# Kernel tuning notes

Hardware: AMD Instinct MI355X
Metric: run time of the kernel (lower is better)

The kernel has to match this reference:

```python
import jax, jax.numpy as jnp
import numpy as np

B, L, D, H = 4, 2048, 1024, 16
HD = D // H  # head_dim = 64


def setup_inputs() -> dict:
    key = jax.random.key(0)
    k1, k2, k3 = jax.random.split(key, 3)
    x = jax.random.normal(k1, (B, L, D), dtype=jnp.float32)
    # causal mask: True where attention is NOT allowed (masked_fill semantics)
    mask = ~jnp.tril(jnp.ones((L, L), dtype=bool))
    Wqkv = jax.random.normal(k2, (3 * D, D), dtype=jnp.float32) * (1.0 / np.sqrt(D))
    bqkv = jnp.zeros((3 * D,), dtype=jnp.float32)
    Wo = jax.random.normal(k3, (D, D), dtype=jnp.float32) * (1.0 / np.sqrt(D))
    bo = jnp.zeros((D,), dtype=jnp.float32)
    return {"x": x, "mask": mask, "Wqkv": Wqkv, "bqkv": bqkv, "Wo": Wo, "bo": bo}


def reference(x, mask, Wqkv, bqkv, Wo, bo):
    b, l, d = x.shape
    qkv = jnp.einsum('bld,ed->ble', x, Wqkv) + bqkv            # [b, l, 3d]
    q, k, v = jnp.split(qkv, 3, axis=-1)
    q = q.reshape(b, l, H, HD).transpose(0, 2, 1, 3)           # [b, h, l, hd]
    k = k.reshape(b, l, H, HD).transpose(0, 2, 1, 3)
    v = v.reshape(b, l, H, HD).transpose(0, 2, 1, 3)
    scale = 1.0 / jnp.sqrt(jnp.float32(HD))
    a = jnp.einsum('bhqd,bhkd->bhqk', q, k) * scale            # [b, h, l, l]
    a = jnp.where(mask, -jnp.inf, a)
    a = jax.nn.softmax(a, axis=-1)
    out = jnp.einsum('bhqk,bhkd->bhqd', a, v)                  # [b, h, l, hd]
    out = out.transpose(0, 2, 1, 3).reshape(b, l, d)
    return jnp.einsum('bld,ed->ble', out, Wo) + bo
```

## Files before the change

kernel.cpp:

```cpp
#include <hip/hip_runtime.h>

typedef __attribute__((ext_vector_type(8))) short short8;
typedef __attribute__((ext_vector_type(4))) float f32x4;
typedef __attribute__((ext_vector_type(16))) float f32x16;
typedef __attribute__((ext_vector_type(2))) int int2v;
typedef __attribute__((ext_vector_type(4))) int int4v;
typedef unsigned short u16;
typedef unsigned int u32;

#define B_ 4
#define L_ 2048
#define D_ 1024
#define H_ 16
#define HD_ 64

__device__ __forceinline__ void load_lds16(const void* g, void* l) {
  __builtin_amdgcn_global_load_lds(
      (__attribute__((address_space(1))) unsigned int*)(g),
      (__attribute__((address_space(3))) unsigned int*)(l),
      16, 0, 0);
}

__device__ __forceinline__ u16 f2bf(float f) {
  union { float f; unsigned u; } c; c.f = f;
  unsigned r = c.u + 0x7FFFu + ((c.u >> 16) & 1u);
  return (u16)(r >> 16);
}

__device__ __forceinline__ u32 cvtpk(float a, float b) {
  u32 r; asm("v_cvt_pk_bf16_f32 %0, %1, %2" : "=v"(r) : "v"(a), "v"(b)); return r;
}

#define TRREAD(dst, base, OFFLIT) \
  asm volatile("ds_read_b64_tr_b16 %0, %1 offset:" OFFLIT : "=v"(dst) : "v"(base))

__device__ __forceinline__ void pswap(u32& a, u32& b) {
  asm("v_permlane32_swap_b32 %0, %1" : "+v"(a), "+v"(b));
}

__global__ __launch_bounds__(256) void cvt_all(const float* __restrict__ x,
                                               const float* __restrict__ wqkv,
                                               const float* __restrict__ wo,
                                               u16* __restrict__ out) {
  const long n1 = (long)B_ * L_ * D_;
  const long n2 = (long)3 * D_ * D_;
  long i = ((long)blockIdx.x * 256 + threadIdx.x) * 4;
  const float* src;
  long off;
  if (i < n1) { src = x; off = i; }
  else if (i < n1 + n2) { src = wqkv; off = i - n1; }
  else { src = wo; off = i - n1 - n2; }
  float4 v = *(const float4*)(src + off);
  u16 o0 = f2bf(v.x), o1 = f2bf(v.y), o2 = f2bf(v.z), o3 = f2bf(v.w);
  u16* p = out + i;
  p[0] = o0; p[1] = o1; p[2] = o2; p[3] = o3;
}

template <int QCOLS, bool BF16_OUT>
__global__ __launch_bounds__(256, 3) void gemm_bt(
    const u16* __restrict__ A, const u16* __restrict__ B,
    const float* __restrict__ bias, void* __restrict__ Cout,
    int M, int N, int K) {
  __shared__ u16 Asm[128 * 64];
  __shared__ u16 Bsm[128 * 64];
  const int tid = threadIdx.x;
  const int lane = tid & 63;
  const int wid = tid >> 6;
  const int fr = lane & 15, fq = lane >> 4;
  const int wr = wid >> 1, wc = wid & 1;

  const int nwg = gridDim.x;
  const int cpx = nwg >> 3;
  const int id = (blockIdx.x & 7) * cpx + (blockIdx.x >> 3);
  const int NBX = N >> 7;
  const long n0 = (long)(id % NBX) * 128;
  const long m0 = (long)(id / NBX) * 128;

  const int srl = lane >> 3;
  const int sgc = ((lane & 7) ^ srl) * 8;

  f32x4 acc[4][4] = {};

  for (int kt = 0; kt < K; kt += 64) {
    __syncthreads();
#pragma unroll
    for (int c = 0; c < 4; ++c) {
      const int row = c * 32 + wid * 8 + srl;
      load_lds16(A + (m0 + row) * K + kt + sgc,
                 (char*)Asm + (c * 256 + wid * 64) * 16);
      load_lds16(B + (n0 + row) * K + kt + sgc,
                 (char*)Bsm + (c * 256 + wid * 64) * 16);
    }
    __syncthreads();
#pragma unroll
    for (int ks = 0; ks < 2; ++ks) {
      short8 af[4], bfr[4];
#pragma unroll
      for (int m = 0; m < 4; ++m) {
        const int row = wr * 64 + m * 16 + fr;
        af[m] = *(const short8*)((const char*)Asm + row * 128 +
                                 (((ks * 4 + fq) ^ (row & 7)) * 16));
      }
#pragma unroll
      for (int n = 0; n < 4; ++n) {
        const int row = wc * 64 + n * 16 + fr;
        bfr[n] = *(const short8*)((const char*)Bsm + row * 128 +
                                  (((ks * 4 + fq) ^ (row & 7)) * 16));
      }
#pragma unroll
      for (int m = 0; m < 4; ++m)
#pragma unroll
        for (int n = 0; n < 4; ++n)
          acc[m][n] = __builtin_amdgcn_mfma_f32_16x16x32_bf16(af[m], bfr[n], acc[m][n], 0, 0, 0);
    }
  }

  float bv[4];
#pragma unroll
  for (int n = 0; n < 4; ++n) bv[n] = bias[n0 + wc * 64 + n * 16 + fr];

#pragma unroll
  for (int m = 0; m < 4; ++m) {
#pragma unroll
    for (int n = 0; n < 4; ++n) {
      const long col = n0 + wc * 64 + n * 16 + fr;
      const float sc = (QCOLS > 0 && col < QCOLS) ? 0.18033688f : 1.0f;
#pragma unroll
      for (int r = 0; r < 4; ++r) {
        const long row = m0 + wr * 64 + m * 16 + fq * 4 + r;
        float v = (acc[m][n][r] + bv[n]) * sc;
        if (BF16_OUT)
          ((u16*)Cout)[row * N + col] = f2bf(v);
        else
          ((float*)Cout)[row * N + col] = v;
      }
    }
  }
}

__global__ __launch_bounds__(256, 4) void flash_attn11(
    const u16* __restrict__ qkv, u16* __restrict__ attn) {
  __shared__ u16 K2[2][64 * 64];
  __shared__ u16 V2[2][64 * 64];

  const int tid = threadIdx.x;
  const int lane = tid & 63;
  const int wid = tid >> 6;
  const int l31 = lane & 31;
  const int h = lane >> 5;

  const int bh = blockIdx.x;
  const int y = blockIdx.y;
  const int qt = (y < 4) ? 15 - y : (y < 8) ? y + 4 : (y < 12) ? 15 - y : y - 12;
  const long rowbase = (long)(bh >> 4) * L_;
  const int hh = bh & 15;

  const int wq0 = qt * 128 + wid * 32;
  const int qg = wq0 + l31;

  short8 qf[4];
  {
    const u16* qp = qkv + (rowbase + qg) * 3072 + hh * 64 + h * 8;
#pragma unroll
    for (int ks = 0; ks < 4; ++ks) qf[ks] = *(const short8*)(qp + ks * 16);
  }

  short8 ones;
#pragma unroll
  for (int j = 0; j < 8; ++j) ones[j] = (short)0x3F80;

  int krow[2], kvv[2], dvv[2];
#pragma unroll
  for (int c = 0; c < 2; ++c) {
    const int s = (wid * 2 + c) * 8 + (lane >> 3);
    krow[c] = s;
    kvv[c] = ((s >> 2) << 2) + ((lane >> 1) & 3);
    dvv[c] = ((s & 3) << 4) + ((lane & 1) << 3);
  }
  const int kchunk = ((lane & 7) ^ (lane >> 3)) * 8;

  const u32 Vaddr = (u32)(unsigned long long)(__attribute__((address_space(3))) char*)(void*)&V2[0][0];
  const u32 vb0 = Vaddr + ((lane >> 4) & 1) * 128 + (lane & 15) * 8 + h * 1024;

  f32x16 o[2] = {};
  float l_r = 0.f;

  auto stage = [&](int kt, int buf) {
    const long ktb = (long)kt * 64;
#pragma unroll
    for (int c = 0; c < 2; ++c) {
      load_lds16(qkv + (rowbase + ktb + krow[c]) * 3072 + 1024 + hh * 64 + kchunk,
                 (char*)&K2[buf][0] + (wid * 2 + c) * 1024);
      load_lds16(qkv + (rowbase + ktb + kvv[c]) * 3072 + 2048 + hh * 64 + dvv[c],
                 (char*)&V2[buf][0] + (wid * 2 + c) * 1024);
    }
  };

  const int ktm = 2 * qt + 1;
  stage(0, 0);
  __syncthreads();
  int cur = 0;
  for (int kt = 0; kt <= ktm; ++kt) {
    if (kt < ktm) stage(kt + 1, cur ^ 1);
    const int ktb = kt * 64;
    if (ktb <= wq0 + 31) {
      const char* Kb = (const char*)&K2[cur][0];
      const u32 vbB = vb0 + (u32)cur * 8192;

      f32x16 p[2];
      __builtin_amdgcn_s_setprio(1);
#pragma unroll
      for (int t = 0; t < 2; ++t) {
        f32x16 acc = {};
#pragma unroll
        for (int ks = 0; ks < 4; ++ks) {
          const int row = t * 32 + l31;
          short8 kf = *(const short8*)(Kb + row * 128 + (((ks * 2 + h) ^ (row & 7)) * 16));
          acc = __builtin_amdgcn_mfma_f32_32x32x16_bf16(kf, qf[ks], acc, 0, 0, 0);
        }
        p[t] = acc;
      }
      __builtin_amdgcn_s_setprio(0);

      __builtin_amdgcn_sched_barrier(0);
      int2v vf[16];
      TRREAD(vf[0], vbB, "0");     TRREAD(vf[1], vbB, "512");
      TRREAD(vf[2], vbB, "2048");  TRREAD(vf[3], vbB, "2560");
      TRREAD(vf[4], vbB, "4096");  TRREAD(vf[5], vbB, "4608");
      TRREAD(vf[6], vbB, "6144");  TRREAD(vf[7], vbB, "6656");
      TRREAD(vf[8], vbB, "256");   TRREAD(vf[9], vbB, "768");
      TRREAD(vf[10], vbB, "2304"); TRREAD(vf[11], vbB, "2816");
      TRREAD(vf[12], vbB, "4352"); TRREAD(vf[13], vbB, "4864");
      TRREAD(vf[14], vbB, "6400"); TRREAD(vf[15], vbB, "6912");

      if (ktb + 63 > wq0) {
#pragma unroll
        for (int t = 0; t < 2; ++t)
#pragma unroll
          for (int r = 0; r < 16; ++r) {
            const int kvg = ktb + t * 32 + (r & 3) + 8 * (r >> 2) + 4 * h;
            p[t][r] = (kvg > qg) ? -__builtin_inff() : p[t][r];
          }
      }

#pragma unroll
      for (int t = 0; t < 2; ++t)
#pragma unroll
        for (int r = 0; r < 16; ++r)
          p[t][r] = __builtin_exp2f(p[t][r]);

      u32 pf[4][4];
#pragma unroll
      for (int t = 0; t < 2; ++t)
#pragma unroll
        for (int ksl = 0; ksl < 2; ++ksl) {
          u32 x0 = cvtpk(p[t][8 * ksl + 0], p[t][8 * ksl + 1]);
          u32 x1 = cvtpk(p[t][8 * ksl + 2], p[t][8 * ksl + 3]);
          u32 y0 = cvtpk(p[t][8 * ksl + 4], p[t][8 * ksl + 5]);
          u32 y1 = cvtpk(p[t][8 * ksl + 6], p[t][8 * ksl + 7]);
          pswap(x0, y0);
          pswap(x1, y1);
          const int ks = t * 2 + ksl;
          pf[ks][0] = x0; pf[ks][1] = x1; pf[ks][2] = y0; pf[ks][3] = y1;
        }

      asm volatile("s_waitcnt lgkmcnt(0)" ::: "memory");
      __builtin_amdgcn_sched_barrier(0);
      __builtin_amdgcn_s_setprio(1);
      f32x16 lac = {};
#pragma unroll
      for (int ks = 0; ks < 4; ++ks) {
        int4v pv;
        pv[0] = (int)pf[ks][0]; pv[1] = (int)pf[ks][1];
        pv[2] = (int)pf[ks][2]; pv[3] = (int)pf[ks][3];
        const short8 pvf = __builtin_bit_cast(short8, pv);
        int4v a0;
        a0[0] = vf[ks * 2][0]; a0[1] = vf[ks * 2][1];
        a0[2] = vf[ks * 2 + 1][0]; a0[3] = vf[ks * 2 + 1][1];
        o[0] = __builtin_amdgcn_mfma_f32_32x32x16_bf16(
            __builtin_bit_cast(short8, a0), pvf, o[0], 0, 0, 0);
        int4v a1;
        a1[0] = vf[8 + ks * 2][0]; a1[1] = vf[8 + ks * 2][1];
        a1[2] = vf[8 + ks * 2 + 1][0]; a1[3] = vf[8 + ks * 2 + 1][1];
        o[1] = __builtin_amdgcn_mfma_f32_32x32x16_bf16(
            __builtin_bit_cast(short8, a1), pvf, o[1], 0, 0, 0);
        lac = __builtin_amdgcn_mfma_f32_32x32x16_bf16(ones, pvf, lac, 0, 0, 0);
      }
      __builtin_amdgcn_s_setprio(0);
      l_r += lac[0];
    }
    __syncthreads();
    cur ^= 1;
  }

  const float invl = 1.0f / l_r;
  u16* orow = attn + (rowbase + qg) * 1024 + hh * 64;
#pragma unroll
  for (int t = 0; t < 2; ++t)
#pragma unroll
    for (int rp = 0; rp < 8; ++rp) {
      const int r0 = rp * 2;
      const u32 w = cvtpk(o[t][r0] * invl, o[t][r0 + 1] * invl);
      const int d = t * 32 + (r0 & 3) + 8 * (r0 >> 2) + 4 * h;
      *(u32*)(orow + d) = w;
    }
}

extern "C" void kernel_launch(void* const* d_in, const int* in_sizes, int n_in,
                              void* d_out, int out_size, void* d_ws, size_t ws_size,
                              hipStream_t stream) {
  const float* x    = (const float*)d_in[0];
  const float* Wqkv = (const float*)d_in[2];
  const float* bqkv = (const float*)d_in[3];
  const float* Wo   = (const float*)d_in[4];
  const float* bo   = (const float*)d_in[5];
  float* out = (float*)d_out;

  const long ML = (long)B_ * L_;
  u16* xb    = (u16*)d_ws;
  u16* wqkvb = xb + ML * D_;
  u16* wob   = wqkvb + (long)3 * D_ * D_;
  u16* qkv   = wob + (long)D_ * D_;
  u16* attn  = qkv + ML * 3 * D_;

  const long ncvt = ML * D_ + (long)3 * D_ * D_ + (long)D_ * D_;
  cvt_all<<<dim3((int)(ncvt / 1024)), 256, 0, stream>>>(x, Wqkv, Wo, xb);

  gemm_bt<1024, true><<<dim3((3 * D_ / 128) * (int)(ML / 128)), 256, 0, stream>>>(
      xb, wqkvb, bqkv, qkv, (int)ML, 3 * D_, D_);

  flash_attn11<<<dim3(64, 16), 256, 0, stream>>>(qkv, attn);

  gemm_bt<0, false><<<dim3((D_ / 128) * (int)(ML / 128)), 256, 0, stream>>>(
      attn, wob, bo, out, (int)ML, D_, D_);
}
```

Baseline: 162.8 us.

## Software-pipeline QK^T of next tile with softmax/PV of previous tile in attention

```diff
diff --git a/kernel.cpp b/kernel.cpp
--- a/kernel.cpp
+++ b/kernel.cpp
@@ -138,10 +138,10 @@
   }
 }
 
-__global__ __launch_bounds__(256, 4) void flash_attn11(
+__global__ __launch_bounds__(256, 2) void flash_attn12(
     const u16* __restrict__ qkv, u16* __restrict__ attn) {
   __shared__ u16 K2[2][64 * 64];
-  __shared__ u16 V2[2][64 * 64];
+  __shared__ u16 V3[3][64 * 64];
 
   const int tid = threadIdx.x;
   const int lane = tid & 63;
@@ -179,121 +179,141 @@
   }
   const int kchunk = ((lane & 7) ^ (lane >> 3)) * 8;
 
-  const u32 Vaddr = (u32)(unsigned long long)(__attribute__((address_space(3))) char*)(void*)&V2[0][0];
+  const u32 Vaddr = (u32)(unsigned long long)(__attribute__((address_space(3))) char*)(void*)&V3[0][0];
   const u32 vb0 = Vaddr + ((lane >> 4) & 1) * 128 + (lane & 15) * 8 + h * 1024;
 
   f32x16 o[2] = {};
-  float l_r = 0.f;
-
-  auto stage = [&](int kt, int buf) {
+  f32x16 lacc = {};
+
+  auto stage = [&](int kt, int kbuf, int vbuf) {
     const long ktb = (long)kt * 64;
 #pragma unroll
     for (int c = 0; c < 2; ++c) {
       load_lds16(qkv + (rowbase + ktb + krow[c]) * 3072 + 1024 + hh * 64 + kchunk,
-                 (char*)&K2[buf][0] + (wid * 2 + c) * 1024);
+                 (char*)&K2[kbuf][0] + (wid * 2 + c) * 1024);
       load_lds16(qkv + (rowbase + ktb + kvv[c]) * 3072 + 2048 + hh * 64 + dvv[c],
-                 (char*)&V2[buf][0] + (wid * 2 + c) * 1024);
+                 (char*)&V3[vbuf][0] + (wid * 2 + c) * 1024);
     }
   };
 
+  auto qk_issue = [&](f32x16& W0, f32x16& W1, int kbuf) {
+    const char* Kb = (const char*)&K2[kbuf][0];
+    __builtin_amdgcn_s_setprio(1);
+#pragma unroll
+    for (int t = 0; t < 2; ++t) {
+      f32x16 acc = {};
+#pragma unroll
+      for (int ks = 0; ks < 4; ++ks) {
+        const int row = t * 32 + l31;
+        short8 kf = *(const short8*)(Kb + row * 128 + (((ks * 2 + h) ^ (row & 7)) * 16));
+        acc = __builtin_amdgcn_mfma_f32_32x32x16_bf16(kf, qf[ks], acc, 0, 0, 0);
+      }
+      if (t == 0) W0 = acc; else W1 = acc;
+    }
+    __builtin_amdgcn_s_setprio(0);
+  };
+
+  auto finish = [&](f32x16& R0, f32x16& R1, int ktbP, int vbuf) {
+    const u32 vbB = vb0 + (u32)vbuf * 8192;
+    int2v vf[16];
+    TRREAD(vf[0], vbB, "0");     TRREAD(vf[1], vbB, "512");
+    TRREAD(vf[2], vbB, "2048");  TRREAD(vf[3], vbB, "2560");
+    TRREAD(vf[4], vbB, "4096");  TRREAD(vf[5], vbB, "4608");
+    TRREAD(vf[6], vbB, "6144");  TRREAD(vf[7], vbB, "6656");
+    TRREAD(vf[8], vbB, "256");   TRREAD(vf[9], vbB, "768");
+    TRREAD(vf[10], vbB, "2304"); TRREAD(vf[11], vbB, "2816");
+    TRREAD(vf[12], vbB, "4352"); TRREAD(vf[13], vbB, "4864");
+    TRREAD(vf[14], vbB, "6400"); TRREAD(vf[15], vbB, "6912");
+
+    f32x16 p[2];
+    p[0] = R0; p[1] = R1;
+    if (ktbP + 63 > wq0) {
+#pragma unroll
+      for (int t = 0; t < 2; ++t)
+#pragma unroll
+        for (int r = 0; r < 16; ++r) {
+          const int kvg = ktbP + t * 32 + (r & 3) + 8 * (r >> 2) + 4 * h;
+          p[t][r] = (kvg > qg) ? -__builtin_inff() : p[t][r];
+        }
+    }
+#pragma unroll
+    for (int t = 0; t < 2; ++t)
+#pragma unroll
+      for (int r = 0; r < 16; ++r)
+        p[t][r] = __builtin_exp2f(p[t][r]);
+
+    u32 pf[4][4];
+#pragma unroll
+    for (int t = 0; t < 2; ++t)
+#pragma unroll
+      for (int ksl = 0; ksl < 2; ++ksl) {
+        u32 x0 = cvtpk(p[t][8 * ksl + 0], p[t][8 * ksl + 1]);
+        u32 x1 = cvtpk(p[t][8 * ksl + 2], p[t][8 * ksl + 3]);
+        u32 y0 = cvtpk(p[t][8 * ksl + 4], p[t][8 * ksl + 5]);
+        u32 y1 = cvtpk(p[t][8 * ksl + 6], p[t][8 * ksl + 7]);
+        pswap(x0, y0);
+        pswap(x1, y1);
+        const int ks = t * 2 + ksl;
+        pf[ks][0] = x0; pf[ks][1] = x1; pf[ks][2] = y0; pf[ks][3] = y1;
+      }
+
+    asm volatile("s_waitcnt lgkmcnt(0)" ::: "memory");
+    __builtin_amdgcn_sched_barrier(0);
+    __builtin_amdgcn_s_setprio(1);
+#pragma unroll
+    for (int ks = 0; ks < 4; ++ks) {
+      int4v pv;
+      pv[0] = (int)pf[ks][0]; pv[1] = (int)pf[ks][1];
+      pv[2] = (int)pf[ks][2]; pv[3] = (int)pf[ks][3];
+      const short8 pvf = __builtin_bit_cast(short8, pv);
+      int4v a0;
+      a0[0] = vf[ks * 2][0]; a0[1] = vf[ks * 2][1];
+      a0[2] = vf[ks * 2 + 1][0]; a0[3] = vf[ks * 2 + 1][1];
+      o[0] = __builtin_amdgcn_mfma_f32_32x32x16_bf16(
+          __builtin_bit_cast(short8, a0), pvf, o[0], 0, 0, 0);
+      int4v a1;
+      a1[0] = vf[8 + ks * 2][0]; a1[1] = vf[8 + ks * 2][1];
+      a1[2] = vf[8 + ks * 2 + 1][0]; a1[3] = vf[8 + ks * 2 + 1][1];
+      o[1] = __builtin_amdgcn_mfma_f32_32x32x16_bf16(
+          __builtin_bit_cast(short8, a1), pvf, o[1], 0, 0, 0);
+      lacc = __builtin_amdgcn_mfma_f32_32x32x16_bf16(ones, pvf, lacc, 0, 0, 0);
+    }
+    __builtin_amdgcn_s_setprio(0);
+  };
+
   const int ktm = 2 * qt + 1;
-  stage(0, 0);
+  stage(0, 0, 0);
   __syncthreads();
-  int cur = 0;
-  for (int kt = 0; kt <= ktm; ++kt) {
-    if (kt < ktm) stage(kt + 1, cur ^ 1);
+
+  f32x16 PA0, PA1, PB0, PB1;
+  int kt = 0, vcur = 0;
+
+  auto step = [&](f32x16& W0, f32x16& W1, f32x16& R0, f32x16& R1) {
     const int ktb = kt * 64;
-    if (ktb <= wq0 + 31) {
-      const char* Kb = (const char*)&K2[cur][0];
-      const u32 vbB = vb0 + (u32)cur * 8192;
-
-      f32x16 p[2];
-      __builtin_amdgcn_s_setprio(1);
-#pragma unroll
-      for (int t = 0; t < 2; ++t) {
-        f32x16 acc = {};
-#pragma unroll
-        for (int ks = 0; ks < 4; ++ks) {
-          const int row = t * 32 + l31;
-          short8 kf = *(const short8*)(Kb + row * 128 + (((ks * 2 + h) ^ (row & 7)) * 16));
-          acc = __builtin_amdgcn_mfma_f32_32x32x16_bf16(kf, qf[ks], acc, 0, 0, 0);
-        }
-        p[t] = acc;
-      }
-      __builtin_amdgcn_s_setprio(0);
-
-      __builtin_amdgcn_sched_barrier(0);
-      int2v vf[16];
-      TRREAD(vf[0], vbB, "0");     TRREAD(vf[1], vbB, "512");
-      TRREAD(vf[2], vbB, "2048");  TRREAD(vf[3], vbB, "2560");
-      TRREAD(vf[4], vbB, "4096");  TRREAD(vf[5], vbB, "4608");
-      TRREAD(vf[6], vbB, "6144");  TRREAD(vf[7], vbB, "6656");
-      TRREAD(vf[8], vbB, "256");   TRREAD(vf[9], vbB, "768");
-      TRREAD(vf[10], vbB, "2304"); TRREAD(vf[11], vbB, "2816");
-      TRREAD(vf[12], vbB, "4352"); TRREAD(vf[13], vbB, "4864");
-      TRREAD(vf[14], vbB, "6400"); TRREAD(vf[15], vbB, "6912");
-
-      if (ktb + 63 > wq0) {
-#pragma unroll
-        for (int t = 0; t < 2; ++t)
-#pragma unroll
-          for (int r = 0; r < 16; ++r) {
-            const int kvg = ktb + t * 32 + (r & 3) + 8 * (r >> 2) + 4 * h;
-            p[t][r] = (kvg > qg) ? -__builtin_inff() : p[t][r];
-          }
-      }
-
-#pragma unroll
-      for (int t = 0; t < 2; ++t)
-#pragma unroll
-        for (int r = 0; r < 16; ++r)
-          p[t][r] = __builtin_exp2f(p[t][r]);
-
-      u32 pf[4][4];
-#pragma unroll
-      for (int t = 0; t < 2; ++t)
-#pragma unroll
-        for (int ksl = 0; ksl < 2; ++ksl) {
-          u32 x0 = cvtpk(p[t][8 * ksl + 0], p[t][8 * ksl + 1]);
-          u32 x1 = cvtpk(p[t][8 * ksl + 2], p[t][8 * ksl + 3]);
-          u32 y0 = cvtpk(p[t][8 * ksl + 4], p[t][8 * ksl + 5]);
-          u32 y1 = cvtpk(p[t][8 * ksl + 6], p[t][8 * ksl + 7]);
-          pswap(x0, y0);
-          pswap(x1, y1);
-          const int ks = t * 2 + ksl;
-          pf[ks][0] = x0; pf[ks][1] = x1; pf[ks][2] = y0; pf[ks][3] = y1;
-        }
-
-      asm volatile("s_waitcnt lgkmcnt(0)" ::: "memory");
-      __builtin_amdgcn_sched_barrier(0);
-      __builtin_amdgcn_s_setprio(1);
-      f32x16 lac = {};
-#pragma unroll
-      for (int ks = 0; ks < 4; ++ks) {
-        int4v pv;
-        pv[0] = (int)pf[ks][0]; pv[1] = (int)pf[ks][1];
-        pv[2] = (int)pf[ks][2]; pv[3] = (int)pf[ks][3];
-        const short8 pvf = __builtin_bit_cast(short8, pv);
-        int4v a0;
-        a0[0] = vf[ks * 2][0]; a0[1] = vf[ks * 2][1];
-        a0[2] = vf[ks * 2 + 1][0]; a0[3] = vf[ks * 2 + 1][1];
-        o[0] = __builtin_amdgcn_mfma_f32_32x32x16_bf16(
-            __builtin_bit_cast(short8, a0), pvf, o[0], 0, 0, 0);
-        int4v a1;
-        a1[0] = vf[8 + ks * 2][0]; a1[1] = vf[8 + ks * 2][1];
-        a1[2] = vf[8 + ks * 2 + 1][0]; a1[3] = vf[8 + ks * 2 + 1][1];
-        o[1] = __builtin_amdgcn_mfma_f32_32x32x16_bf16(
-            __builtin_bit_cast(short8, a1), pvf, o[1], 0, 0, 0);
-        lac = __builtin_amdgcn_mfma_f32_32x32x16_bf16(ones, pvf, lac, 0, 0, 0);
-      }
-      __builtin_amdgcn_s_setprio(0);
-      l_r += lac[0];
-    }
-    __syncthreads();
-    cur ^= 1;
-  }
-
-  const float invl = 1.0f / l_r;
+    if (kt <= ktm) {
+      if (kt < ktm) {
+        const int vn = (vcur == 2) ? 0 : vcur + 1;
+        stage(kt + 1, (kt + 1) & 1, vn);
+      }
+      if (ktb <= wq0 + 31) qk_issue(W0, W1, kt & 1);
+    }
+    if (kt >= 1 && (ktb - 64) <= wq0 + 31) {
+      const int vp = (vcur == 0) ? 2 : vcur - 1;
+      finish(R0, R1, ktb - 64, vp);
+    }
+    if (kt <= ktm) __syncthreads();
+  };
+
+  while (true) {
+    step(PA0, PA1, PB0, PB1);
+    if (kt == ktm + 1) break;
+    ++kt; vcur = (vcur == 2) ? 0 : vcur + 1;
+    step(PB0, PB1, PA0, PA1);
+    if (kt == ktm + 1) break;
+    ++kt; vcur = (vcur == 2) ? 0 : vcur + 1;
+  }
+
+  const float invl = 1.0f / lacc[0];
   u16* orow = attn + (rowbase + qg) * 1024 + hh * 64;
 #pragma unroll
   for (int t = 0; t < 2; ++t)
@@ -329,7 +349,7 @@
   gemm_bt<1024, true><<<dim3((3 * D_ / 128) * (int)(ML / 128)), 256, 0, stream>>>(
       xb, wqkvb, bqkv, qkv, (int)ML, 3 * D_, D_);
 
-  flash_attn11<<<dim3(64, 16), 256, 0, stream>>>(qkv, attn);
+  flash_attn12<<<dim3(64, 16), 256, 0, stream>>>(qkv, attn);
 
   gemm_bt<0, false><<<dim3((D_ / 128) * (int)(ML / 128)), 256, 0, stream>>>(
       attn, wob, bo, out, (int)ML, D_, D_);
```

Measured after the change: 160.5 us. Within noise of the previous version (-1.4%).

## Replace direct global-to-LDS loads with register-staged prefetch in GEMM and attention

Applied to the files above, without the earlier changes.

```diff
diff --git a/kernel.cpp b/kernel.cpp
--- a/kernel.cpp
+++ b/kernel.cpp
@@ -14,12 +14,6 @@
 #define H_ 16
 #define HD_ 64
 
-__device__ __forceinline__ void load_lds16(const void* g, void* l) {
-  __builtin_amdgcn_global_load_lds(
-      (__attribute__((address_space(1))) unsigned int*)(g),
-      (__attribute__((address_space(3))) unsigned int*)(l),
-      16, 0, 0);
-}
 
 __device__ __forceinline__ u16 f2bf(float f) {
   union { float f; unsigned u; } c; c.f = f;
@@ -32,7 +26,8 @@
 }
 
 #define TRREAD(dst, base, OFFLIT) \
-  asm volatile("ds_read_b64_tr_b16 %0, %1 offset:" OFFLIT : "=v"(dst) : "v"(base))
+  asm volatile("ds_read_b64_tr_b16 %0, %1 offset:" OFFLIT \
+               : "=v"(dst) : "v"(base) : "memory")
 
 __device__ __forceinline__ void pswap(u32& a, u32& b) {
   asm("v_permlane32_swap_b32 %0, %1" : "+v"(a), "+v"(b));
@@ -79,19 +74,40 @@
   const int srl = lane >> 3;
   const int sgc = ((lane & 7) ^ srl) * 8;
 
+  const u16* gA[4];
+  const u16* gB[4];
+  u32 ldst[4];
+#pragma unroll
+  for (int c = 0; c < 4; ++c) {
+    const int row = c * 32 + wid * 8 + srl;
+    gA[c] = A + (m0 + row) * K + sgc;
+    gB[c] = B + (n0 + row) * K + sgc;
+    ldst[c] = (u32)((c * 256 + wid * 64) * 16 + lane * 16);
+  }
+
   f32x4 acc[4][4] = {};
+  short8 rA[4], rB[4];
+#pragma unroll
+  for (int c = 0; c < 4; ++c) {
+    rA[c] = *(const short8*)(gA[c]);
+    rB[c] = *(const short8*)(gB[c]);
+  }
 
   for (int kt = 0; kt < K; kt += 64) {
     __syncthreads();
 #pragma unroll
     for (int c = 0; c < 4; ++c) {
-      const int row = c * 32 + wid * 8 + srl;
-      load_lds16(A + (m0 + row) * K + kt + sgc,
-                 (char*)Asm + (c * 256 + wid * 64) * 16);
-      load_lds16(B + (n0 + row) * K + kt + sgc,
-                 (char*)Bsm + (c * 256 + wid * 64) * 16);
+      *(short8*)((char*)Asm + ldst[c]) = rA[c];
+      *(short8*)((char*)Bsm + ldst[c]) = rB[c];
     }
     __syncthreads();
+    if (kt + 64 < K) {
+#pragma unroll
+      for (int c = 0; c < 4; ++c) {
+        rA[c] = *(const short8*)(gA[c] + kt + 64);
+        rB[c] = *(const short8*)(gB[c] + kt + 64);
+      }
+    }
 #pragma unroll
     for (int ks = 0; ks < 2; ++ks) {
       short8 af[4], bfr[4];
@@ -138,10 +154,10 @@
   }
 }
 
-__global__ __launch_bounds__(256, 4) void flash_attn11(
+__global__ __launch_bounds__(256, 4) void flash_attn18(
     const u16* __restrict__ qkv, u16* __restrict__ attn) {
-  __shared__ u16 K2[2][64 * 64];
-  __shared__ u16 V2[2][64 * 64];
+  __shared__ u16 K1[64 * 64];
+  __shared__ u16 V1[64 * 64];
 
   const int tid = threadIdx.x;
   const int lane = tid & 63;
@@ -169,43 +185,53 @@
 #pragma unroll
   for (int j = 0; j < 8; ++j) ones[j] = (short)0x3F80;
 
-  int krow[2], kvv[2], dvv[2];
+  const u16* gK[2];
+  const u16* gV[2];
+  u32 dstKV[2];
 #pragma unroll
   for (int c = 0; c < 2; ++c) {
     const int s = (wid * 2 + c) * 8 + (lane >> 3);
-    krow[c] = s;
-    kvv[c] = ((s >> 2) << 2) + ((lane >> 1) & 3);
-    dvv[c] = ((s & 3) << 4) + ((lane & 1) << 3);
-  }
-  const int kchunk = ((lane & 7) ^ (lane >> 3)) * 8;
-
-  const u32 Vaddr = (u32)(unsigned long long)(__attribute__((address_space(3))) char*)(void*)&V2[0][0];
+    const int kvv = ((s >> 2) << 2) + ((lane >> 1) & 3);
+    const int dvv = ((s & 3) << 4) + ((lane & 1) << 3);
+    const int kchunk = ((lane & 7) ^ (lane >> 3)) * 8;
+    gK[c] = qkv + (rowbase + s) * 3072 + 1024 + hh * 64 + kchunk;
+    gV[c] = qkv + (rowbase + kvv) * 3072 + 2048 + hh * 64 + dvv;
+    dstKV[c] = (u32)((wid * 2 + c) * 1024 + lane * 16);
+  }
+
+  const u32 Vaddr = (u32)(unsigned long long)(__attribute__((address_space(3))) char*)(void*)&V1[0];
   const u32 vb0 = Vaddr + ((lane >> 4) & 1) * 128 + (lane & 15) * 8 + h * 1024;
 
   f32x16 o[2] = {};
   float l_r = 0.f;
 
-  auto stage = [&](int kt, int buf) {
-    const long ktb = (long)kt * 64;
+  short8 stK[2], stV[2];
+#pragma unroll
+  for (int c = 0; c < 2; ++c) {
+    stK[c] = *(const short8*)(gK[c]);
+    stV[c] = *(const short8*)(gV[c]);
+  }
+
+  const int ktm = 2 * qt + 1;
+  for (int kt = 0; kt <= ktm; ++kt) {
+    __syncthreads();
 #pragma unroll
     for (int c = 0; c < 2; ++c) {
-      load_lds16(qkv + (rowbase + ktb + krow[c]) * 3072 + 1024 + hh * 64 + kchunk,
-                 (char*)&K2[buf][0] + (wid * 2 + c) * 1024);
-      load_lds16(qkv + (rowbase + ktb + kvv[c]) * 3072 + 2048 + hh * 64 + dvv[c],
-                 (char*)&V2[buf][0] + (wid * 2 + c) * 1024);
-    }
-  };
-
-  const int ktm = 2 * qt + 1;
-  stage(0, 0);
-  __syncthreads();
-  int cur = 0;
-  for (int kt = 0; kt <= ktm; ++kt) {
-    if (kt < ktm) stage(kt + 1, cur ^ 1);
+      *(short8*)((char*)K1 + dstKV[c]) = stK[c];
+      *(short8*)((char*)V1 + dstKV[c]) = stV[c];
+    }
+    __syncthreads();
+    if (kt < ktm) {
+      const long goff = (long)(kt + 1) * 64 * 3072;
+#pragma unroll
+      for (int c = 0; c < 2; ++c) {
+        stK[c] = *(const short8*)(gK[c] + goff);
+        stV[c] = *(const short8*)(gV[c] + goff);
+      }
+    }
     const int ktb = kt * 64;
     if (ktb <= wq0 + 31) {
-      const char* Kb = (const char*)&K2[cur][0];
-      const u32 vbB = vb0 + (u32)cur * 8192;
+      const char* Kb = (const char*)K1;
 
       f32x16 p[2];
       __builtin_amdgcn_s_setprio(1);
@@ -224,14 +250,14 @@
 
       __builtin_amdgcn_sched_barrier(0);
       int2v vf[16];
-      TRREAD(vf[0], vbB, "0");     TRREAD(vf[1], vbB, "512");
-      TRREAD(vf[2], vbB, "2048");  TRREAD(vf[3], vbB, "2560");
-      TRREAD(vf[4], vbB, "4096");  TRREAD(vf[5], vbB, "4608");
-      TRREAD(vf[6], vbB, "6144");  TRREAD(vf[7], vbB, "6656");
-      TRREAD(vf[8], vbB, "256");   TRREAD(vf[9], vbB, "768");
-      TRREAD(vf[10], vbB, "2304"); TRREAD(vf[11], vbB, "2816");
-      TRREAD(vf[12], vbB, "4352"); TRREAD(vf[13], vbB, "4864");
-      TRREAD(vf[14], vbB, "6400"); TRREAD(vf[15], vbB, "6912");
+      TRREAD(vf[0], vb0, "0");     TRREAD(vf[1], vb0, "512");
+      TRREAD(vf[2], vb0, "2048");  TRREAD(vf[3], vb0, "2560");
+      TRREAD(vf[4], vb0, "4096");  TRREAD(vf[5], vb0, "4608");
+      TRREAD(vf[6], vb0, "6144");  TRREAD(vf[7], vb0, "6656");
+      TRREAD(vf[8], vb0, "256");   TRREAD(vf[9], vb0, "768");
+      TRREAD(vf[10], vb0, "2304"); TRREAD(vf[11], vb0, "2816");
+      TRREAD(vf[12], vb0, "4352"); TRREAD(vf[13], vb0, "4864");
+      TRREAD(vf[14], vb0, "6400"); TRREAD(vf[15], vb0, "6912");
 
       if (ktb + 63 > wq0) {
 #pragma unroll
@@ -289,8 +315,6 @@
       __builtin_amdgcn_s_setprio(0);
       l_r += lac[0];
     }
-    __syncthreads();
-    cur ^= 1;
   }
 
   const float invl = 1.0f / l_r;
@@ -329,7 +353,7 @@
   gemm_bt<1024, true><<<dim3((3 * D_ / 128) * (int)(ML / 128)), 256, 0, stream>>>(
       xb, wqkvb, bqkv, qkv, (int)ML, 3 * D_, D_);
 
-  flash_attn11<<<dim3(64, 16), 256, 0, stream>>>(qkv, attn);
+  flash_attn18<<<dim3(64, 16), 256, 0, stream>>>(qkv, attn);
 
   gemm_bt<0, false><<<dim3((D_ / 128) * (int)(ML / 128)), 256, 0, stream>>>(
       attn, wob, bo, out, (int)ML, D_, D_);
```

Result: slower. 191.4 us (+17.6%).
